# Performance work log

Measured on AMD Instinct MI355X. Metric: run time of the kernel, lower is better.

Reference implementation:

```python
import jax, jax.numpy as jnp
import numpy as np

N_NODES = 50000
E = 800000
D = 64
H = 128


def _ln(x, g, b, eps=1e-5):
    m = x.mean(-1, keepdims=True)
    v = ((x - m) ** 2).mean(-1, keepdims=True)
    return (x - m) * jax.lax.rsqrt(v + eps) * g + b


def setup_inputs() -> dict:
    key = jax.random.key(0)
    ks = jax.random.split(key, 8)
    return dict(
        node_emb=jax.random.normal(ks[0], (N_NODES, D), jnp.float32),
        src=jax.random.randint(ks[1], (E,), 0, N_NODES),
        dst=jax.random.randint(ks[2], (E,), 0, N_NODES),
        noise=jax.random.uniform(ks[3], (E,), jnp.float32, 1e-6, 1.0 - 1e-6),
        W1=jax.random.normal(ks[4], (2 * D, H), jnp.float32) * 0.05,
        b1=jnp.zeros((H,), jnp.float32),
        g1=jnp.ones((H,), jnp.float32),
        bt1=jnp.zeros((H,), jnp.float32),
        W2=jax.random.normal(ks[5], (H, H // 2), jnp.float32) * 0.05,
        b2=jnp.zeros((H // 2,), jnp.float32),
        g2=jnp.ones((H // 2,), jnp.float32),
        bt2=jnp.zeros((H // 2,), jnp.float32),
        W3=jax.random.normal(ks[6], (H // 2, 1), jnp.float32) * 0.05,
        b3=jnp.zeros((1,), jnp.float32),
    )


def reference(node_emb, src, dst, noise, W1, b1, g1, bt1, W2, b2, g2, bt2, W3, b3):
    # edge gather + concat: [E, 2D]
    edge_emb = jnp.concatenate([node_emb[src], node_emb[dst]], axis=1)
    # edge MLP with LayerNorm + relu (dropout=0 / eval)
    h = jax.nn.relu(_ln(edge_emb @ W1 + b1, g1, bt1))
    h = jax.nn.relu(_ln(h @ W2 + b2, g2, bt2))
    logit = (h @ W3 + b3).reshape(-1)  # [E]
    # concrete gate, bias=0, beta=1.0 (forward default)
    beta = 1.0
    gate = jax.nn.sigmoid((jnp.log(noise) - jnp.log1p(-noise) + logit) / beta)
    # degree norm: out_deg(src)^-1/2 * in_deg(dst)^-1/2, degrees clamped to >=1
    ones = jnp.ones((src.shape[0],), node_emb.dtype)
    out_deg = jnp.maximum(jax.ops.segment_sum(ones, src, num_segments=N_NODES), 1.0)
    in_deg = jnp.maximum(jax.ops.segment_sum(ones, dst, num_segments=N_NODES), 1.0)
    norm = jax.lax.rsqrt(out_deg)[src] * jax.lax.rsqrt(in_deg)[dst]
    return gate * norm
```

## Files before the change

kernel.cpp:

```cpp
#include <hip/hip_runtime.h>
#include <hip/hip_bf16.h>

#define N_NODES 50000
#define NE      800000
#define NT32    (NE / 32)
#define NTILES  (NE / 16)

typedef __attribute__((ext_vector_type(8)))  short bf16x8;
typedef __attribute__((ext_vector_type(4)))  float f32x4;
typedef __attribute__((ext_vector_type(16))) float f32x16;
typedef __attribute__((ext_vector_type(4)))  int   i32x4;
typedef __attribute__((ext_vector_type(2)))  int   i32x2;

static __device__ __forceinline__ short f2bf(float x) {
    union { float f; unsigned u; } v; v.f = x;
    unsigned r = (v.u + 0x7fffu + ((v.u >> 16) & 1u)) >> 16;
    return (short)r;
}
static __device__ __forceinline__ float bflo(unsigned u) {
    union { unsigned u; float f; } v; v.u = u << 16; return v.f;
}
static __device__ __forceinline__ float bfhi(unsigned u) {
    union { unsigned u; float f; } v; v.u = u & 0xffff0000u; return v.f;
}
static __device__ __forceinline__ float bfs(unsigned short u) {
    union { unsigned u; float f; } v; v.u = ((unsigned)u) << 16; return v.f;
}

#define OFF_W2   32768
#define OFF_B1   49152
#define OFF_B2   49408
#define OFF_GT1  49536
#define OFF_GT2  50048
#define OFF_W3   50304
#define IMG_B    50432
#define IMG_V4   (IMG_B / 16)


__global__ void prep_hist(const float* __restrict__ emb,
                          const int* __restrict__ src, const int* __restrict__ dst,
                          const float* __restrict__ W1, const float* __restrict__ b1,
                          const float* __restrict__ g1, const float* __restrict__ bt1,
                          const float* __restrict__ W2, const float* __restrict__ b2,
                          const float* __restrict__ g2, const float* __restrict__ bt2,
                          const float* __restrict__ W3,
                          ushort* __restrict__ embB, char* __restrict__ img,
                          int* __restrict__ outd, int* __restrict__ ind)
{
    const int i0 = blockIdx.x * 256 + threadIdx.x;
    const int n  = gridDim.x * 256;

    for (int t = i0; t < (N_NODES * 64 / 8); t += n) {
        const f32x4* p = (const f32x4*)(emb + (size_t)t * 8);
        f32x4 a = p[0], b = p[1];
        unsigned u0 = (unsigned)(ushort)f2bf(a[0]) | ((unsigned)(ushort)f2bf(a[1]) << 16);
        unsigned u1 = (unsigned)(ushort)f2bf(a[2]) | ((unsigned)(ushort)f2bf(a[3]) << 16);
        unsigned u2 = (unsigned)(ushort)f2bf(b[0]) | ((unsigned)(ushort)f2bf(b[1]) << 16);
        unsigned u3 = (unsigned)(ushort)f2bf(b[2]) | ((unsigned)(ushort)f2bf(b[3]) << 16);
        i32x4 o = {(int)u0, (int)u1, (int)u2, (int)u3};
        *(i32x4*)(embB + (size_t)t * 8) = o;
    }
    for (int t = i0; t < NE; t += n) {
        atomicAdd(outd + src[t], 1);
        atomicAdd(ind + dst[t], 1);
    }
    ushort* W1f = (ushort*)img;
    for (int t = i0; t < 16384; t += n) {
        int j = t & 7, lane = (t >> 3) & 63, f = t >> 9;
        int mt = f >> 3, ke = f & 7, h = lane >> 5, c = lane & 31;
        W1f[t] = f2bf(W1[(16 * ke + 8 * h + j) * 128 + 32 * mt + c]);
    }
    ushort* W2f = (ushort*)(img + OFF_W2);
    for (int t = i0; t < 8192; t += n) {
        int j = t & 7, lane = (t >> 3) & 63, f = t >> 9;
        int mt = f >> 3, ke = f & 7, h = lane >> 5, c = lane & 31;
        W2f[t] = f2bf(W2[(16 * ke + 8 * h + j) * 64 + 32 * mt + c]);
    }
    if (i0 < 128) ((ushort*)(img + OFF_B1))[i0] = f2bf(b1[i0]);
    if (i0 < 64)  ((ushort*)(img + OFF_B2))[i0] = f2bf(b2[i0]);
    if (i0 < 128) {
        int r4 = i0 & 3, h = (i0 >> 2) & 1, q4 = (i0 >> 3) & 3, mt = i0 >> 5;
        int f = 32 * mt + 8 * q4 + 4 * h + r4;
        ((unsigned*)(img + OFF_GT1))[i0] =
            (unsigned)(ushort)f2bf(g1[f]) | ((unsigned)(ushort)f2bf(bt1[f]) << 16);
    }
    if (i0 < 64) {
        int r4 = i0 & 3, h = (i0 >> 2) & 1, q4 = (i0 >> 3) & 3, mt = i0 >> 5;
        int f = 32 * mt + 8 * q4 + 4 * h + r4;
        ((unsigned*)(img + OFF_GT2))[i0] =
            (unsigned)(ushort)f2bf(g2[f]) | ((unsigned)(ushort)f2bf(bt2[f]) << 16);
        ((ushort*)(img + OFF_W3))[i0] = f2bf(W3[f]);
    }
}


__global__ __launch_bounds__(256, 3) void edge_mlp32(
    const ushort* __restrict__ embB,
    const int*   __restrict__ src, const int* __restrict__ dst,
    const float* __restrict__ noise,
    const i32x4* __restrict__ WFimg,
    const float* __restrict__ b3p,
    const int* __restrict__ outd, const int* __restrict__ ind,
    float* __restrict__ out)
{
    __shared__ i32x4 ldsv[IMG_V4];
    char* ldsb = (char*)ldsv;

    const int tid = threadIdx.x;
    for (int i = tid; i < IMG_V4; i += 256) ldsv[i] = WFimg[i];
    __syncthreads();

    const int wid = tid >> 6;
    const int l   = tid & 63;
    const int h   = l >> 5;
    const int c   = l & 31;

    const float b3v = b3p[0];

    bf16x8 bone = {};
    bone[0] = (h == 0) ? (short)0x3F80 : (short)0;

    const int gw = blockIdx.x * 4 + wid;
    const int nw = gridDim.x * 4;

    for (int tile = gw; tile < NT32; tile += nw) {
        unsigned tz;
        asm volatile("v_mov_b32 %0, 0" : "=v"(tz));
        const char* ldz = ldsb + tz;

        const int e0 = tile * 32 + c;
        const int sn = src[e0], dn = dst[e0];

        const ushort* sp = embB + (size_t)sn * 64;
        const ushort* dp = embB + (size_t)dn * 64;
        bf16x8 bf[8];
#pragma unroll
        for (int ke = 0; ke < 4; ++ke) bf[ke]     = *(const bf16x8*)(sp + 16 * ke + 8 * h);
#pragma unroll
        for (int ke = 0; ke < 4; ++ke) bf[4 + ke] = *(const bf16x8*)(dp + 16 * ke + 8 * h);

        const ushort* W1z = (const ushort*)ldz;
        f32x16 acc[4] = {};
#pragma unroll
        for (int ke = 0; ke < 8; ++ke) {
#pragma unroll
            for (int mt = 0; mt < 4; ++mt) {
                bf16x8 w = *(const bf16x8*)(W1z + (mt * 8 + ke) * 512 + l * 8);
                acc[mt] = __builtin_amdgcn_mfma_f32_32x32x16_bf16(w, bf[ke], acc[mt], 0, 0, 0);
            }
        }
        const ushort* b1z = (const ushort*)(ldz + OFF_B1);
#pragma unroll
        for (int mt = 0; mt < 4; ++mt) {
            bf16x8 w = {};
            short bv = b1z[32 * mt + c];
            w[0] = (h == 0) ? bv : (short)0;
            acc[mt] = __builtin_amdgcn_mfma_f32_32x32x16_bf16(w, bone, acc[mt], 0, 0, 0);
        }

        float s0 = 0.f, s1 = 0.f, q0 = 0.f, q1 = 0.f;
#pragma unroll
        for (int mt = 0; mt < 4; ++mt) {
#pragma unroll
            for (int i = 0; i < 16; i += 2) {
                float v0 = acc[mt][i], v1 = acc[mt][i + 1];
                s0 += v0; q0 = fmaf(v0, v0, q0);
                s1 += v1; q1 = fmaf(v1, v1, q1);
            }
        }
        float s = s0 + s1, q = q0 + q1;
        s += __shfl_xor(s, 32);
        q += __shfl_xor(q, 32);
        const float mu = s * (1.0f / 128.0f);
        const float rs = rsqrtf(q * (1.0f / 128.0f) - mu * mu + 1e-5f);
        const float c0 = -mu * rs;

        const ushort* W2z = (const ushort*)(ldz + OFF_W2);
        f32x16 acc2[2] = {};
#pragma unroll
        for (int mt = 0; mt < 4; ++mt) {
            unsigned pk[4][2];
#pragma unroll
            for (int q4 = 0; q4 < 4; ++q4) {
                i32x4 pg = *(const i32x4*)(ldz + OFF_GT1 + ((mt * 4 + q4) * 2 + h) * 16);
                float t[4];
#pragma unroll
                for (int r4 = 0; r4 < 4; ++r4) {
                    unsigned u = (unsigned)pg[r4];
                    float v = acc[mt][q4 * 4 + r4];
                    float w = fmaf(v, rs, c0);
                    float y = fmaf(w, bflo(u), bfhi(u));
                    t[r4] = fmaxf(y, 0.f);
                }
                pk[q4][0] = (unsigned)(ushort)f2bf(t[0]) | ((unsigned)(ushort)f2bf(t[1]) << 16);
                pk[q4][1] = (unsigned)(ushort)f2bf(t[2]) | ((unsigned)(ushort)f2bf(t[3]) << 16);
            }
#pragma unroll
            for (int sub = 0; sub < 2; ++sub) {
                const int ke = 2 * mt + sub;
                const int qa = 2 * sub, qb = qa + 1;
                unsigned S0 = h ? pk[qa][0] : pk[qb][0];
                unsigned S1 = h ? pk[qa][1] : pk[qb][1];
                unsigned r0 = (unsigned)__shfl_xor((int)S0, 32);
                unsigned r1 = (unsigned)__shfl_xor((int)S1, 32);
                unsigned o0 = h ? pk[qb][0] : pk[qa][0];
                unsigned o1 = h ? pk[qb][1] : pk[qa][1];
                union { i32x4 i; bf16x8 b; } u;
                u.i[0] = (int)(h ? r0 : o0);
                u.i[1] = (int)(h ? r1 : o1);
                u.i[2] = (int)(h ? o0 : r0);
                u.i[3] = (int)(h ? o1 : r1);
#pragma unroll
                for (int mt2 = 0; mt2 < 2; ++mt2) {
                    bf16x8 w = *(const bf16x8*)(W2z + (mt2 * 8 + ke) * 512 + l * 8);
                    acc2[mt2] = __builtin_amdgcn_mfma_f32_32x32x16_bf16(w, u.b, acc2[mt2], 0, 0, 0);
                }
            }
        }
        const ushort* b2z = (const ushort*)(ldz + OFF_B2);
#pragma unroll
        for (int mt2 = 0; mt2 < 2; ++mt2) {
            bf16x8 w = {};
            short bv = b2z[32 * mt2 + c];
            w[0] = (h == 0) ? bv : (short)0;
            acc2[mt2] = __builtin_amdgcn_mfma_f32_32x32x16_bf16(w, bone, acc2[mt2], 0, 0, 0);
        }

        float t0 = 0.f, t1 = 0.f, p0 = 0.f, p1 = 0.f;
#pragma unroll
        for (int mt2 = 0; mt2 < 2; ++mt2) {
#pragma unroll
            for (int i = 0; i < 16; i += 2) {
                float v0 = acc2[mt2][i], v1 = acc2[mt2][i + 1];
                t0 += v0; p0 = fmaf(v0, v0, p0);
                t1 += v1; p1 = fmaf(v1, v1, p1);
            }
        }
        float s2 = t0 + t1, q2 = p0 + p1;
        s2 += __shfl_xor(s2, 32);
        q2 += __shfl_xor(q2, 32);
        const float mu2 = s2 * (1.0f / 64.0f);
        const float rs2 = rsqrtf(q2 * (1.0f / 64.0f) - mu2 * mu2 + 1e-5f);
        const float c02 = -mu2 * rs2;

        float lg = 0.f;
#pragma unroll
        for (int mt2 = 0; mt2 < 2; ++mt2) {
#pragma unroll
            for (int q4 = 0; q4 < 4; ++q4) {
                const int bse = (mt2 * 4 + q4) * 2 + h;
                i32x4 pg = *(const i32x4*)(ldz + OFF_GT2 + bse * 16);
                i32x2 wq = *(const i32x2*)(ldz + OFF_W3 + bse * 8);
#pragma unroll
                for (int r4 = 0; r4 < 4; ++r4) {
                    unsigned ug = (unsigned)pg[r4];
                    unsigned short uw = (unsigned short)(((unsigned)wq[r4 >> 1]) >> (16 * (r4 & 1)));
                    float v = acc2[mt2][q4 * 4 + r4];
                    float w = fmaf(v, rs2, c02);
                    float y = fmaf(w, bflo(ug), bfhi(ug));
                    y = fmaxf(y, 0.f);
                    lg = fmaf(y, bfs(uw), lg);
                }
            }
        }
        lg += __shfl_xor(lg, 32);
        lg += b3v;

        if (h == 0) {
            float nz = noise[e0];
            float z = __logf(nz) - log1pf(-nz) + lg;
            float gate = 1.0f / (1.0f + __expf(-z));
            int od = outd[sn]; if (od < 1) od = 1;
            int idg = ind[dn]; if (idg < 1) idg = 1;
            out[e0] = gate * (rsqrtf((float)od) * rsqrtf((float)idg));
        }
    }
}


__global__ void degree_hist(const int* __restrict__ src, const int* __restrict__ dst,
                            int* __restrict__ outd, int* __restrict__ ind) {
    int i = blockIdx.x * 256 + threadIdx.x;
    if (i < NE) {
        atomicAdd(outd + src[i], 1);
        atomicAdd(ind + dst[i], 1);
    }
}

__global__ __launch_bounds__(256, 2) void edge_mlp_mfma(
    const float* __restrict__ emb,
    const int*   __restrict__ src, const int* __restrict__ dst,
    const float* __restrict__ noise,
    const float* __restrict__ W1, const float* __restrict__ b1,
    const float* __restrict__ g1, const float* __restrict__ bt1,
    const float* __restrict__ W2, const float* __restrict__ b2,
    const float* __restrict__ g2, const float* __restrict__ bt2,
    const float* __restrict__ W3, const float* __restrict__ b3,
    const int*   __restrict__ outd, const int* __restrict__ ind,
    float* __restrict__ out)
{
    __shared__ short lds[32768];
    const int tid = threadIdx.x;
    const int wid = tid >> 6;
    const int l   = tid & 63;
    const int g   = l >> 4;
    const int c   = l & 15;

    for (int i = tid; i < 16384; i += 256) {
        int j = i & 7, lane = (i >> 3) & 63, p = i >> 9;
        int ks = p >> 3, t = p & 7;
        int row = ks * 32 + (lane >> 4) * 8 + j;
        int col = t * 16 + (lane & 15);
        lds[i] = f2bf(W1[row * 128 + col]);
    }
    for (int i = tid; i < 8192; i += 256) {
        int j = i & 7, lane = (i >> 3) & 63, p = i >> 9;
        int ks = p >> 2, t = p & 3;
        int row = ks * 32 + (lane >> 4) * 8 + j;
        int col = t * 16 + (lane & 15);
        lds[16384 + i] = f2bf(W2[row * 64 + col]);
    }
    __syncthreads();

    short* Hl = lds + 24576 + wid * 2048;
    float b1v[8], g1v[8], t1v[8];
#pragma unroll
    for (int t = 0; t < 8; ++t) { int f = t * 16 + c; b1v[t] = b1[f]; g1v[t] = g1[f]; t1v[t] = bt1[f]; }
    float b2v[4], g2v[4], t2v[4], w3v[4];
#pragma unroll
    for (int t = 0; t < 4; ++t) { int f = t * 16 + c; b2v[t] = b2[f]; g2v[t] = g2[f]; t2v[t] = bt2[f]; w3v[t] = W3[f]; }
    const float b3v = b3[0];

    const int gw = blockIdx.x * 4 + wid;
    const int nw = gridDim.x * 4;

    for (int tile = gw; tile < NTILES; tile += nw) {
        const int e0 = tile * 16 + c;
        const int sn = src[e0], dn = dst[e0];
        const f32x4* sp = (const f32x4*)(emb + (size_t)sn * 64);
        const f32x4* dp = (const f32x4*)(emb + (size_t)dn * 64);
        f32x4 u[8];
        u[0] = sp[2 * g]; u[1] = sp[2 * g + 1];
        u[2] = sp[8 + 2 * g]; u[3] = sp[8 + 2 * g + 1];
        u[4] = dp[2 * g]; u[5] = dp[2 * g + 1];
        u[6] = dp[8 + 2 * g]; u[7] = dp[8 + 2 * g + 1];

        bf16x8 a1[4];
#pragma unroll
        for (int ks = 0; ks < 4; ++ks) {
            f32x4 x0 = u[2 * ks], x1 = u[2 * ks + 1];
            bf16x8 a;
            a[0] = f2bf(x0[0]); a[1] = f2bf(x0[1]); a[2] = f2bf(x0[2]); a[3] = f2bf(x0[3]);
            a[4] = f2bf(x1[0]); a[5] = f2bf(x1[1]); a[6] = f2bf(x1[2]); a[7] = f2bf(x1[3]);
            a1[ks] = a;
        }
        f32x4 acc1[8];
#pragma unroll
        for (int t = 0; t < 8; ++t) { f32x4 z = {b1v[t], b1v[t], b1v[t], b1v[t]}; acc1[t] = z; }
#pragma unroll
        for (int ks = 0; ks < 4; ++ks) {
#pragma unroll
            for (int t = 0; t < 8; ++t) {
                bf16x8 b = *(const bf16x8*)(lds + (ks * 8 + t) * 512 + l * 8);
                acc1[t] = __builtin_amdgcn_mfma_f32_16x16x32_bf16(a1[ks], b, acc1[t], 0, 0, 0);
            }
        }
        float mean[4], rstd[4];
#pragma unroll
        for (int r = 0; r < 4; ++r) {
            float s = acc1[0][r];
#pragma unroll
            for (int t = 1; t < 8; ++t) s += acc1[t][r];
            s += __shfl_xor(s, 1); s += __shfl_xor(s, 2);
            s += __shfl_xor(s, 4); s += __shfl_xor(s, 8);
            float m = s * (1.0f / 128.0f);
            float q = 0.f;
#pragma unroll
            for (int t = 0; t < 8; ++t) { float d = acc1[t][r] - m; q = fmaf(d, d, q); }
            q += __shfl_xor(q, 1); q += __shfl_xor(q, 2);
            q += __shfl_xor(q, 4); q += __shfl_xor(q, 8);
            mean[r] = m; rstd[r] = rsqrtf(q * (1.0f / 128.0f) + 1e-5f);
        }
#pragma unroll
        for (int r = 0; r < 4; ++r) {
            int rw = g * 4 + r;
            int swz = (rw & 7) << 3;
#pragma unroll
            for (int t = 0; t < 8; ++t) {
                float y = fmaf((acc1[t][r] - mean[r]) * rstd[r], g1v[t], t1v[t]);
                y = fmaxf(y, 0.f);
                Hl[rw * 128 + ((t * 16 + c) ^ swz)] = f2bf(y);
            }
        }
        bf16x8 a2[4];
        const int swzr = (c & 7) << 3;
#pragma unroll
        for (int ks = 0; ks < 4; ++ks)
            a2[ks] = *(const bf16x8*)(Hl + c * 128 + ((ks * 32 + g * 8) ^ swzr));

        f32x4 acc2[4];
#pragma unroll
        for (int t = 0; t < 4; ++t) { f32x4 z = {b2v[t], b2v[t], b2v[t], b2v[t]}; acc2[t] = z; }
#pragma unroll
        for (int ks = 0; ks < 4; ++ks) {
#pragma unroll
            for (int t = 0; t < 4; ++t) {
                bf16x8 b = *(const bf16x8*)(lds + 16384 + (ks * 4 + t) * 512 + l * 8);
                acc2[t] = __builtin_amdgcn_mfma_f32_16x16x32_bf16(a2[ks], b, acc2[t], 0, 0, 0);
            }
        }
        float logit[4];
#pragma unroll
        for (int r = 0; r < 4; ++r) {
            float s = acc2[0][r] + acc2[1][r] + acc2[2][r] + acc2[3][r];
            s += __shfl_xor(s, 1); s += __shfl_xor(s, 2);
            s += __shfl_xor(s, 4); s += __shfl_xor(s, 8);
            float m = s * (1.0f / 64.0f);
            float q = 0.f;
#pragma unroll
            for (int t = 0; t < 4; ++t) { float d = acc2[t][r] - m; q = fmaf(d, d, q); }
            q += __shfl_xor(q, 1); q += __shfl_xor(q, 2);
            q += __shfl_xor(q, 4); q += __shfl_xor(q, 8);
            float rs = rsqrtf(q * (1.0f / 64.0f) + 1e-5f);
            float p = 0.f;
#pragma unroll
            for (int t = 0; t < 4; ++t) {
                float y = fmaf((acc2[t][r] - m) * rs, g2v[t], t2v[t]);
                y = fmaxf(y, 0.f);
                p = fmaf(y, w3v[t], p);
            }
            p += __shfl_xor(p, 1); p += __shfl_xor(p, 2);
            p += __shfl_xor(p, 4); p += __shfl_xor(p, 8);
            logit[r] = p + b3v;
        }
        if (c < 4) {
            int e = tile * 16 + g * 4 + c;
            float lg = (c == 0) ? logit[0] : (c == 1) ? logit[1] : (c == 2) ? logit[2] : logit[3];
            float nz = noise[e];
            float z = __logf(nz) - log1pf(-nz) + lg;
            float gate = 1.0f / (1.0f + __expf(-z));
            int od = outd[src[e]]; if (od < 1) od = 1;
            int idg = ind[dst[e]]; if (idg < 1) idg = 1;
            out[e] = gate * (rsqrtf((float)od) * rsqrtf((float)idg));
        }
    }
}


extern "C" void kernel_launch(void* const* d_in, const int* in_sizes, int n_in,
                              void* d_out, int out_size, void* d_ws, size_t ws_size,
                              hipStream_t stream) {
    const float* emb   = (const float*)d_in[0];
    const int*   src   = (const int*)  d_in[1];
    const int*   dst   = (const int*)  d_in[2];
    const float* noise = (const float*)d_in[3];
    const float* W1  = (const float*)d_in[4];
    const float* b1  = (const float*)d_in[5];
    const float* g1  = (const float*)d_in[6];
    const float* bt1 = (const float*)d_in[7];
    const float* W2  = (const float*)d_in[8];
    const float* b2  = (const float*)d_in[9];
    const float* g2  = (const float*)d_in[10];
    const float* bt2 = (const float*)d_in[11];
    const float* W3  = (const float*)d_in[12];
    const float* b3  = (const float*)d_in[13];

    char* ws = (char*)d_ws;
    const size_t NEED = 6400000 + IMG_B + 400000;

    if (ws_size >= NEED) {
        ushort* embB = (ushort*)ws;
        char*   img  = ws + 6400000;
        int* outd = (int*)(ws + 6400000 + IMG_B);
        int* ind  = outd + N_NODES;

        hipMemsetAsync(outd, 0, 2 * N_NODES * sizeof(int), stream);
        prep_hist<<<1024, 256, 0, stream>>>(emb, src, dst, W1, b1, g1, bt1,
                                            W2, b2, g2, bt2, W3,
                                            embB, img, outd, ind);
        edge_mlp32<<<768, 256, 0, stream>>>(embB, src, dst, noise, (const i32x4*)img,
                                            b3, outd, ind, (float*)d_out);
    } else {
        int* outd = (int*)ws;
        int* ind  = outd + N_NODES;
        hipMemsetAsync(outd, 0, 2 * N_NODES * sizeof(int), stream);
        degree_hist<<<(NE + 255) / 256, 256, 0, stream>>>(src, dst, outd, ind);
        edge_mlp_mfma<<<512, 256, 0, stream>>>(emb, src, dst, noise,
                                               W1, b1, g1, bt1,
                                               W2, b2, g2, bt2,
                                               W3, b3, outd, ind,
                                               (float*)d_out);
    }
}
```

Measured before the change: 156.9 us.

## Software-prefetch next tile's gathered embeddings and split degree histogram kernel

The edge MLP kernel now prefetches the next tile's src/dst indices and gathered bf16 embedding rows partway through the layer-2 MFMA loop. This hides gather latency behind compute instead of stalling at the top of each tile. The degree histogram moves out of the prep kernel into its own fully parallel launch, and bf16 packing switches to the hardware packed-convert intrinsic. The prefetch raises register pressure at 3 waves per SIMD, and the extra launch adds a small fixed cost.

```diff
diff --git a/kernel.cpp b/kernel.cpp
--- a/kernel.cpp
+++ b/kernel.cpp
@@ -25,6 +25,12 @@
 }
 static __device__ __forceinline__ float bfs(unsigned short u) {
     union { unsigned u; float f; } v; v.u = ((unsigned)u) << 16; return v.f;
+}
+static __device__ __forceinline__ unsigned pk2bf(float a, float b) {
+    union { __hip_bfloat162 h; unsigned u; } v;
+    float2 f; f.x = a; f.y = b;
+    v.h = __float22bfloat162_rn(f);
+    return v.u;
 }
 
 #define OFF_W2   32768
@@ -37,15 +43,13 @@
 #define IMG_V4   (IMG_B / 16)
 
 
-__global__ void prep_hist(const float* __restrict__ emb,
-                          const int* __restrict__ src, const int* __restrict__ dst,
-                          const float* __restrict__ W1, const float* __restrict__ b1,
-                          const float* __restrict__ g1, const float* __restrict__ bt1,
-                          const float* __restrict__ W2, const float* __restrict__ b2,
-                          const float* __restrict__ g2, const float* __restrict__ bt2,
-                          const float* __restrict__ W3,
-                          ushort* __restrict__ embB, char* __restrict__ img,
-                          int* __restrict__ outd, int* __restrict__ ind)
+__global__ void pack_consts(const float* __restrict__ emb,
+                            const float* __restrict__ W1, const float* __restrict__ b1,
+                            const float* __restrict__ g1, const float* __restrict__ bt1,
+                            const float* __restrict__ W2, const float* __restrict__ b2,
+                            const float* __restrict__ g2, const float* __restrict__ bt2,
+                            const float* __restrict__ W3,
+                            ushort* __restrict__ embB, char* __restrict__ img)
 {
     const int i0 = blockIdx.x * 256 + threadIdx.x;
     const int n  = gridDim.x * 256;
@@ -53,16 +57,12 @@
     for (int t = i0; t < (N_NODES * 64 / 8); t += n) {
         const f32x4* p = (const f32x4*)(emb + (size_t)t * 8);
         f32x4 a = p[0], b = p[1];
-        unsigned u0 = (unsigned)(ushort)f2bf(a[0]) | ((unsigned)(ushort)f2bf(a[1]) << 16);
-        unsigned u1 = (unsigned)(ushort)f2bf(a[2]) | ((unsigned)(ushort)f2bf(a[3]) << 16);
-        unsigned u2 = (unsigned)(ushort)f2bf(b[0]) | ((unsigned)(ushort)f2bf(b[1]) << 16);
-        unsigned u3 = (unsigned)(ushort)f2bf(b[2]) | ((unsigned)(ushort)f2bf(b[3]) << 16);
+        unsigned u0 = pk2bf(a[0], a[1]);
+        unsigned u1 = pk2bf(a[2], a[3]);
+        unsigned u2 = pk2bf(b[0], b[1]);
+        unsigned u3 = pk2bf(b[2], b[3]);
         i32x4 o = {(int)u0, (int)u1, (int)u2, (int)u3};
         *(i32x4*)(embB + (size_t)t * 8) = o;
-    }
-    for (int t = i0; t < NE; t += n) {
-        atomicAdd(outd + src[t], 1);
-        atomicAdd(ind + dst[t], 1);
     }
     ushort* W1f = (ushort*)img;
     for (int t = i0; t < 16384; t += n) {
@@ -90,6 +90,16 @@
         ((unsigned*)(img + OFF_GT2))[i0] =
             (unsigned)(ushort)f2bf(g2[f]) | ((unsigned)(ushort)f2bf(bt2[f]) << 16);
         ((ushort*)(img + OFF_W3))[i0] = f2bf(W3[f]);
+    }
+}
+
+
+__global__ void degree_hist(const int* __restrict__ src, const int* __restrict__ dst,
+                            int* __restrict__ outd, int* __restrict__ ind) {
+    int i = blockIdx.x * 256 + threadIdx.x;
+    if (i < NE) {
+        atomicAdd(outd + src[i], 1);
+        atomicAdd(ind + dst[i], 1);
     }
 }
 
@@ -123,30 +133,51 @@
     const int gw = blockIdx.x * 4 + wid;
     const int nw = gridDim.x * 4;
 
+    int sn, dn;
+    bf16x8 fA0, fA1, fA2, fA3, fB0, fB1, fB2, fB3;
+    {
+        int t0 = (gw < NT32) ? gw : (NT32 - 1);
+        int e0p = t0 * 32 + c;
+        sn = src[e0p]; dn = dst[e0p];
+        const ushort* sp = embB + (size_t)sn * 64;
+        const ushort* dp = embB + (size_t)dn * 64;
+        fA0 = *(const bf16x8*)(sp + 8 * h);
+        fA1 = *(const bf16x8*)(sp + 16 + 8 * h);
+        fA2 = *(const bf16x8*)(sp + 32 + 8 * h);
+        fA3 = *(const bf16x8*)(sp + 48 + 8 * h);
+        fB0 = *(const bf16x8*)(dp + 8 * h);
+        fB1 = *(const bf16x8*)(dp + 16 + 8 * h);
+        fB2 = *(const bf16x8*)(dp + 32 + 8 * h);
+        fB3 = *(const bf16x8*)(dp + 48 + 8 * h);
+    }
+
     for (int tile = gw; tile < NT32; tile += nw) {
         unsigned tz;
         asm volatile("v_mov_b32 %0, 0" : "=v"(tz));
         const char* ldz = ldsb + tz;
 
         const int e0 = tile * 32 + c;
-        const int sn = src[e0], dn = dst[e0];
-
-        const ushort* sp = embB + (size_t)sn * 64;
-        const ushort* dp = embB + (size_t)dn * 64;
-        bf16x8 bf[8];
-#pragma unroll
-        for (int ke = 0; ke < 4; ++ke) bf[ke]     = *(const bf16x8*)(sp + 16 * ke + 8 * h);
-#pragma unroll
-        for (int ke = 0; ke < 4; ++ke) bf[4 + ke] = *(const bf16x8*)(dp + 16 * ke + 8 * h);
+
+        const int tn  = tile + nw;
+        const int tcl = (tn < NT32) ? tn : tile;
+        const int e0n = tcl * 32 + c;
+        int snN = src[e0n];
+        int dnN = dst[e0n];
+        float nz = noise[e0];
+        int odv = outd[sn];
+        int idv = ind[dn];
 
         const ushort* W1z = (const ushort*)ldz;
         f32x16 acc[4] = {};
-#pragma unroll
-        for (int ke = 0; ke < 8; ++ke) {
-#pragma unroll
-            for (int mt = 0; mt < 4; ++mt) {
-                bf16x8 w = *(const bf16x8*)(W1z + (mt * 8 + ke) * 512 + l * 8);
-                acc[mt] = __builtin_amdgcn_mfma_f32_32x32x16_bf16(w, bf[ke], acc[mt], 0, 0, 0);
+        {
+            bf16x8 bfr[8] = {fA0, fA1, fA2, fA3, fB0, fB1, fB2, fB3};
+#pragma unroll
+            for (int ke = 0; ke < 8; ++ke) {
+#pragma unroll
+                for (int mt = 0; mt < 4; ++mt) {
+                    bf16x8 w = *(const bf16x8*)(W1z + (mt * 8 + ke) * 512 + l * 8);
+                    acc[mt] = __builtin_amdgcn_mfma_f32_32x32x16_bf16(w, bfr[ke], acc[mt], 0, 0, 0);
+                }
             }
         }
         const ushort* b1z = (const ushort*)(ldz + OFF_B1);
@@ -192,8 +223,8 @@
                     float y = fmaf(w, bflo(u), bfhi(u));
                     t[r4] = fmaxf(y, 0.f);
                 }
-                pk[q4][0] = (unsigned)(ushort)f2bf(t[0]) | ((unsigned)(ushort)f2bf(t[1]) << 16);
-                pk[q4][1] = (unsigned)(ushort)f2bf(t[2]) | ((unsigned)(ushort)f2bf(t[3]) << 16);
+                pk[q4][0] = pk2bf(t[0], t[1]);
+                pk[q4][1] = pk2bf(t[2], t[3]);
             }
 #pragma unroll
             for (int sub = 0; sub < 2; ++sub) {
@@ -216,6 +247,18 @@
                     acc2[mt2] = __builtin_amdgcn_mfma_f32_32x32x16_bf16(w, u.b, acc2[mt2], 0, 0, 0);
                 }
             }
+            if (mt == 1) {
+                const ushort* spn = embB + (size_t)snN * 64;
+                const ushort* dpn = embB + (size_t)dnN * 64;
+                fA0 = *(const bf16x8*)(spn + 8 * h);
+                fA1 = *(const bf16x8*)(spn + 16 + 8 * h);
+                fA2 = *(const bf16x8*)(spn + 32 + 8 * h);
+                fA3 = *(const bf16x8*)(spn + 48 + 8 * h);
+                fB0 = *(const bf16x8*)(dpn + 8 * h);
+                fB1 = *(const bf16x8*)(dpn + 16 + 8 * h);
+                fB2 = *(const bf16x8*)(dpn + 32 + 8 * h);
+                fB3 = *(const bf16x8*)(dpn + 48 + 8 * h);
+            }
         }
         const ushort* b2z = (const ushort*)(ldz + OFF_B2);
 #pragma unroll
@@ -267,25 +310,17 @@
         lg += b3v;
 
         if (h == 0) {
-            float nz = noise[e0];
             float z = __logf(nz) - log1pf(-nz) + lg;
             float gate = 1.0f / (1.0f + __expf(-z));
-            int od = outd[sn]; if (od < 1) od = 1;
-            int idg = ind[dn]; if (idg < 1) idg = 1;
+            int od = odv; if (od < 1) od = 1;
+            int idg = idv; if (idg < 1) idg = 1;
             out[e0] = gate * (rsqrtf((float)od) * rsqrtf((float)idg));
         }
-    }
-}
-
-
-__global__ void degree_hist(const int* __restrict__ src, const int* __restrict__ dst,
-                            int* __restrict__ outd, int* __restrict__ ind) {
-    int i = blockIdx.x * 256 + threadIdx.x;
-    if (i < NE) {
-        atomicAdd(outd + src[i], 1);
-        atomicAdd(ind + dst[i], 1);
-    }
-}
+
+        sn = snN; dn = dnN;
+    }
+}
+
 
 __global__ __launch_bounds__(256, 2) void edge_mlp_mfma(
     const float* __restrict__ emb,
@@ -475,9 +510,9 @@
         int* ind  = outd + N_NODES;
 
         hipMemsetAsync(outd, 0, 2 * N_NODES * sizeof(int), stream);
-        prep_hist<<<1024, 256, 0, stream>>>(emb, src, dst, W1, b1, g1, bt1,
-                                            W2, b2, g2, bt2, W3,
-                                            embB, img, outd, ind);
+        pack_consts<<<1024, 256, 0, stream>>>(emb, W1, b1, g1, bt1,
+                                              W2, b2, g2, bt2, W3, embB, img);
+        degree_hist<<<(NE + 255) / 256, 256, 0, stream>>>(src, dst, outd, ind);
         edge_mlp32<<<768, 256, 0, stream>>>(embB, src, dst, noise, (const i32x4*)img,
                                             b3, outd, ind, (float*)d_out);
     } else {
```

New measurement: 159.6 us. About the same (+1.7%).
